# Optimization experiments

Hardware: AMD Instinct MI355X
Metric: run time of the kernel (lower is better)

Reference implementation:

```python
import jax, jax.numpy as jnp
import numpy as np

DIM = 1024
HEADS = 16
SCALE = DIM ** -0.5  # note: source scales by full dim, not head dim


def setup_inputs() -> dict:
    key = jax.random.key(0)
    k1, k2, k3 = jax.random.split(key, 3)
    b, n = 2, 2048
    x = jax.random.normal(k1, (b, n, DIM), dtype=jnp.float32)
    w_qkv = jax.random.normal(k2, (3 * DIM, DIM), dtype=jnp.float32) * (DIM ** -0.5)
    w_out = jax.random.normal(k3, (DIM, DIM), dtype=jnp.float32) * (DIM ** -0.5)
    b_out = jnp.zeros((DIM,), dtype=jnp.float32)
    return {"x": x, "w_qkv": w_qkv, "w_out": w_out, "b_out": b_out}


def reference(x, w_qkv, w_out, b_out):
    b, n, d = x.shape
    h = HEADS
    hd = d // h
    # torch Linear: y = x @ W.T
    qkv = x @ w_qkv.T  # [b, n, 3d]
    q, k, v = jnp.split(qkv, 3, axis=-1)
    # reshape to [b, h, n, hd]
    def to_heads(t):
        return t.reshape(b, n, h, hd).transpose(0, 2, 1, 3)
    q, k, v = to_heads(q), to_heads(k), to_heads(v)
    dots = jnp.einsum('bhqd,bhkd->bhqk', q, k) * SCALE
    attn = jax.nn.softmax(dots, axis=-1)
    out = jnp.einsum('bhqk,bhkd->bhqd', attn, v)
    out = out.transpose(0, 2, 1, 3).reshape(b, n, d)
    return out @ w_out.T + b_out
```

## Files before the change

### kernel.cpp

```cpp
#include <hip/hip_runtime.h>

typedef __attribute__((ext_vector_type(8))) _Float16 half8;
typedef __attribute__((ext_vector_type(4))) _Float16 half4;
typedef __attribute__((ext_vector_type(2))) __fp16 fp16x2;
typedef __attribute__((ext_vector_type(4))) float f32x4;
typedef __attribute__((ext_vector_type(4))) unsigned int u32x4;
typedef __attribute__((ext_vector_type(2))) unsigned int u32x2;

#define NSEQ 2048
#define DIMM 1024
#define NH   16
#define HD   64

typedef const void __attribute__((address_space(1))) gvoid_t;
typedef void __attribute__((address_space(3))) svoid_t;

__device__ __forceinline__ void gload_lds16(const void* g, void* l) {
  __builtin_amdgcn_global_load_lds((gvoid_t*)g, (svoid_t*)l, 16, 0, 0);
}

union H2U { fp16x2 h; unsigned int u; };

__global__ __launch_bounds__(256) void cvt_all(const float* __restrict__ x,
                                               const float* __restrict__ wqkv,
                                               const float* __restrict__ wout,
                                               _Float16* __restrict__ xh,
                                               _Float16* __restrict__ wqkvh,
                                               _Float16* __restrict__ wouth) {
  int i = blockIdx.x * 256 + threadIdx.x;
  const float* src;
  _Float16* dst;
  int off;
  if (i < 524288) { src = x; dst = xh; off = i; }
  else if (i < 917504) { src = wqkv; dst = wqkvh; off = i - 524288; }
  else { src = wout; dst = wouth; off = i - 917504; }
  const float4* p = (const float4*)src + (size_t)off * 2;
  float4 v0 = p[0], v1 = p[1];
  half8 h;
  h[0] = (_Float16)v0.x; h[1] = (_Float16)v0.y; h[2] = (_Float16)v0.z; h[3] = (_Float16)v0.w;
  h[4] = (_Float16)v1.x; h[5] = (_Float16)v1.y; h[6] = (_Float16)v1.z; h[7] = (_Float16)v1.w;
  *((half8*)dst + off) = h;
}

__device__ __forceinline__ void gemm_mainloop(const _Float16* __restrict__ A,
                                              const _Float16* __restrict__ B,
                                              int am0, int bn0,
                                              _Float16* As, _Float16* Bs,
                                              f32x4 acc[4][4]) {
  const int tid = threadIdx.x;
  const int w = tid >> 6, lane = tid & 63;
  const int lr = lane >> 2;
  const int lc = (lane & 3) * 8;
  const int wm = (w >> 1) * 64, wn = (w & 1) * 64;
  const int g = lane >> 4, ln = lane & 15;

  for (int k0 = 0; k0 < 1024; k0 += 32) {
#pragma unroll
    for (int rr = 0; rr < 4; ++rr) {
      int c = rr * 4 + w;
      if (c < 8) {
        gload_lds16(A + (size_t)(am0 + c * 16 + lr) * 1024 + k0 + lc, As + c * 512);
      } else {
        int cb = c - 8;
        gload_lds16(B + (size_t)(bn0 + cb * 16 + lr) * 1024 + k0 + lc, Bs + cb * 512);
      }
    }
    __syncthreads();
    half8 af[4], bf[4];
#pragma unroll
    for (int mi = 0; mi < 4; ++mi)
      af[mi] = *(const half8*)(As + (wm + mi * 16 + ln) * 32 + g * 8);
#pragma unroll
    for (int ni = 0; ni < 4; ++ni)
      bf[ni] = *(const half8*)(Bs + (wn + ni * 16 + ln) * 32 + g * 8);
#pragma unroll
    for (int mi = 0; mi < 4; ++mi)
#pragma unroll
      for (int ni = 0; ni < 4; ++ni)
        acc[mi][ni] = __builtin_amdgcn_mfma_f32_16x16x32_f16(af[mi], bf[ni], acc[mi][ni], 0, 0, 0);
    __syncthreads();
  }
}

union SmemQKV {
  struct { _Float16 a[128 * 32]; _Float16 b[128 * 32]; } ab;
  _Float16 t[128 * 136];
};

#define QSCALE 0.0450843450f

__global__ __launch_bounds__(256) void gemm_qkv(const _Float16* __restrict__ x,
                                                const _Float16* __restrict__ wqkv,
                                                _Float16* __restrict__ qh,
                                                _Float16* __restrict__ kh,
                                                _Float16* __restrict__ vt) {
  __shared__ SmemQKV sh;
  f32x4 acc[4][4];
#pragma unroll
  for (int i = 0; i < 4; ++i)
#pragma unroll
    for (int j = 0; j < 4; ++j) acc[i][j] = (f32x4){0.f, 0.f, 0.f, 0.f};
  const int bm = blockIdx.x, bn = blockIdx.y;
  gemm_mainloop(x, wqkv, bm * 128, bn * 128, sh.ab.a, sh.ab.b, acc);

  const int tid = threadIdx.x;
  const int w = tid >> 6, lane = tid & 63;
  const int g = lane >> 4, ln = lane & 15;
  const int wm = (w >> 1) * 64, wn = (w & 1) * 64;
  const int sec = bn >> 3;
  const int cbase = (bn & 7) * 128;

  if (sec < 2) {
    _Float16* dst = (sec == 0) ? qh : kh;
    const float scale = (sec == 0) ? QSCALE : 1.0f;
#pragma unroll
    for (int mi = 0; mi < 4; ++mi) {
      int row = bm * 128 + wm + mi * 16 + g * 4;
      int bidx = row >> 11, nidx = row & 2047;
#pragma unroll
      for (int ni = 0; ni < 4; ++ni) {
        int col = cbase + wn + ni * 16 + ln;
        int h = col >> 6, d = col & 63;
        _Float16* p = dst + ((size_t)(bidx * NH + h) * NSEQ + nidx) * HD + d;
#pragma unroll
        for (int r = 0; r < 4; ++r) p[r * HD] = (_Float16)(acc[mi][ni][r] * scale);
      }
    }
  } else {
    __syncthreads();
#pragma unroll
    for (int mi = 0; mi < 4; ++mi)
#pragma unroll
      for (int ni = 0; ni < 4; ++ni)
#pragma unroll
        for (int r = 0; r < 4; ++r)
          sh.t[(wn + ni * 16 + ln) * 136 + wm + mi * 16 + g * 4 + r] = (_Float16)acc[mi][ni][r];
    __syncthreads();
    const int row0 = bm * 128;
    const int bidx = row0 >> 11, n0 = row0 & 2047;
#pragma unroll
    for (int i = 0; i < 8; ++i) {
      int ci = i * 256 + tid;
      int drow = ci >> 4, nofs = (ci & 15) * 8;
      int col = cbase + drow;
      int h = col >> 6, d = col & 63;
      u32x4 val = *(const u32x4*)(sh.t + drow * 136 + nofs);
      *(u32x4*)(vt + ((size_t)(bidx * NH + h) * HD + d) * NSEQ + n0 + nofs) = val;
    }
  }
}

__global__ __launch_bounds__(256, 2) void attn_fwd(const _Float16* __restrict__ qg,
                                                   const _Float16* __restrict__ kg,
                                                   const _Float16* __restrict__ vg,
                                                   _Float16* __restrict__ ao) {
  __shared__ _Float16 Ks[3][64 * 64];
  __shared__ _Float16 Vs[3][64 * 64];
  __shared__ float Lred[2][128];

  const int bid = blockIdx.x;
  const int swz = (bid & 7) * 64 + (bid >> 3);
  const int bh = swz >> 4, qt = swz & 15;
  const int tid = threadIdx.x, w = tid >> 6, lane = tid & 63;
  const int g = lane >> 4, ln = lane & 15;
  const int sw8 = ln & 7;
  const int qh2 = w >> 1, kh2 = w & 1;

  const _Float16* qp = qg + (size_t)bh * NSEQ * HD;
  const _Float16* kp = kg + (size_t)bh * NSEQ * HD;
  const _Float16* vp = vg + (size_t)bh * HD * NSEQ;

  const int qr0 = qt * 128;

  half8 qf[4][2];
#pragma unroll
  for (int qb = 0; qb < 4; ++qb)
#pragma unroll
    for (int dk = 0; dk < 2; ++dk)
      qf[qb][dk] = *(const half8*)(qp + (size_t)(qr0 + qh2 * 64 + qb * 16 + ln) * HD + dk * 32 + g * 8);
  asm volatile("" ::: "memory");

  const int rsub = lane >> 3;
  const int csw = ((lane & 7) ^ rsub) << 3;
  const int c0 = 2 * w;
  const int R0 = c0 * 8 + rsub, R1 = R0 + 8;
  const int ks0 = 32 * (R0 >> 5) + 8 * ((R0 >> 2) & 3) + 4 * ((R0 >> 4) & 1) + (R0 & 3);
  const int ks1 = 32 * (R1 >> 5) + 8 * ((R1 >> 2) & 3) + 4 * ((R1 >> 4) & 1) + (R1 & 3);

#define STAGE(buf, tt)                                                              \
  {                                                                                 \
    const _Float16* kt_ = kp + (size_t)(tt) * 64 * HD;                              \
    gload_lds16(kt_ + (size_t)ks0 * HD + csw, &Ks[buf][c0 * 512]);                  \
    gload_lds16(kt_ + (size_t)ks1 * HD + csw, &Ks[buf][(c0 + 1) * 512]);            \
    gload_lds16(vp + (size_t)(c0 * 8 + rsub) * NSEQ + (tt) * 64 + csw,              \
                &Vs[buf][c0 * 512]);                                                \
    gload_lds16(vp + (size_t)((c0 + 1) * 8 + rsub) * NSEQ + (tt) * 64 + csw,        \
                &Vs[buf][(c0 + 1) * 512]);                                          \
  }

  STAGE(0, 0);
  STAGE(1, 1);

  float lsum[4] = {0.f, 0.f, 0.f, 0.f};
  f32x4 oacc[4][4];
#pragma unroll
  for (int sd = 0; sd < 4; ++sd)
#pragma unroll
    for (int qb = 0; qb < 4; ++qb) oacc[sd][qb] = (f32x4){0.f, 0.f, 0.f, 0.f};
  const f32x4 fz = (f32x4){0.f, 0.f, 0.f, 0.f};

#define TILE_BODY(kbuf, vbuf)                                                       \
  {                                                                                 \
    const _Float16* kb_ = (kbuf);                                                   \
    const _Float16* vb_ = (vbuf);                                                   \
    f32x4 sacc[2][4];                                                  \
    __builtin_amdgcn_s_setprio(1);                                                  \
    _Pragma("unroll")                                                               \
    for (int s = 0; s < 2; ++s) {                                                   \
      const _Float16* kr = kb_ + (kh2 * 32 + s * 16 + ln) * 64;                     \
      half8 kf0 = *(const half8*)(kr + ((g ^ sw8) << 3));                           \
      half8 kf1 = *(const half8*)(kr + (((4 + g) ^ sw8) << 3));                     \
      _Pragma("unroll")                                                             \
      for (int qb = 0; qb < 4; ++qb) {                                              \
        sacc[s][qb] = __builtin_amdgcn_mfma_f32_16x16x32_f16(kf0, qf[qb][0], fz, 0, 0, 0);          \
        sacc[s][qb] = __builtin_amdgcn_mfma_f32_16x16x32_f16(kf1, qf[qb][1], sacc[s][qb], 0, 0, 0); \
      }                                                                             \
    }                                                                               \
    __builtin_amdgcn_s_setprio(0);                                                  \
    half8 vf[4];                          \
    _Pragma("unroll")                                                               \
    for (int sd = 0; sd < 4; ++sd)                                                  \
      vf[sd] = *(const half8*)(vb_ + (sd * 16 + ln) * 64 +                          \
                               (((kh2 * 4 + g) ^ sw8) << 3));                       \
    half8 pb[4];                                                                    \
    _Pragma("unroll")                                                               \
    for (int qb = 0; qb < 4; ++qb) {                                                \
      float e0 = __builtin_amdgcn_exp2f(sacc[0][qb][0]);                            \
      float e1 = __builtin_amdgcn_exp2f(sacc[0][qb][1]);                            \
      float e2 = __builtin_amdgcn_exp2f(sacc[0][qb][2]);                            \
      float e3 = __builtin_amdgcn_exp2f(sacc[0][qb][3]);                            \
      float e4 = __builtin_amdgcn_exp2f(sacc[1][qb][0]);                            \
      float e5 = __builtin_amdgcn_exp2f(sacc[1][qb][1]);                            \
      float e6 = __builtin_amdgcn_exp2f(sacc[1][qb][2]);                            \
      float e7 = __builtin_amdgcn_exp2f(sacc[1][qb][3]);                            \
      lsum[qb] += ((e0 + e1) + (e2 + e3)) + ((e4 + e5) + (e6 + e7));                \
      H2U c0_, c1_, c2_, c3_;                                                       \
      c0_.h = __builtin_amdgcn_cvt_pkrtz(e0, e1);                                   \
      c1_.h = __builtin_amdgcn_cvt_pkrtz(e2, e3);                                   \
      c2_.h = __builtin_amdgcn_cvt_pkrtz(e4, e5);                                   \
      c3_.h = __builtin_amdgcn_cvt_pkrtz(e6, e7);                                   \
      union { u32x4 u; half8 h; } pk;                                               \
      pk.u[0] = c0_.u; pk.u[1] = c1_.u; pk.u[2] = c2_.u; pk.u[3] = c3_.u;           \
      pb[qb] = pk.h;                                                                \
    }                                                                               \
    __builtin_amdgcn_s_setprio(1);                                                  \
    _Pragma("unroll")                                                               \
    for (int sd = 0; sd < 4; ++sd)                                                  \
      _Pragma("unroll")                                                             \
      for (int qb = 0; qb < 4; ++qb)                                                \
        oacc[sd][qb] = __builtin_amdgcn_mfma_f32_16x16x32_f16(vf[sd], pb[qb], oacc[sd][qb], 0, 0, 0); \
    __builtin_amdgcn_s_setprio(0);                                                  \
  }

  for (int t = 0; t < 30; ++t) {
    asm volatile("s_waitcnt vmcnt(4)" ::: "memory");
    __builtin_amdgcn_s_barrier();
    STAGE((t + 2) % 3, t + 2);
    TILE_BODY(&Ks[t % 3][0], &Vs[t % 3][0])
  }
  {
    asm volatile("s_waitcnt vmcnt(4)" ::: "memory");
    __builtin_amdgcn_s_barrier();
    TILE_BODY(&Ks[0][0], &Vs[0][0])
  }
  {
    asm volatile("s_waitcnt vmcnt(0)" ::: "memory");
    __builtin_amdgcn_s_barrier();
    TILE_BODY(&Ks[1][0], &Vs[1][0])
  }

#pragma unroll
  for (int qb = 0; qb < 4; ++qb) {
    lsum[qb] += __shfl_xor(lsum[qb], 16, 64);
    lsum[qb] += __shfl_xor(lsum[qb], 32, 64);
  }
  __syncthreads();
  float* Osh = (float*)&Ks[0][0];
  if (g == 0) {
#pragma unroll
    for (int qb = 0; qb < 4; ++qb)
      Lred[kh2][qh2 * 64 + qb * 16 + ln] = lsum[qb];
  }
  if (kh2) {
#pragma unroll
    for (int sd = 0; sd < 4; ++sd)
#pragma unroll
      for (int qb = 0; qb < 4; ++qb)
        *(f32x4*)&Osh[(qh2 * 64 + qb * 16 + ln) * 66 + sd * 16 + g * 4] = oacc[sd][qb];
  }
  __syncthreads();
  if (!kh2) {
    const int bidx = bh >> 4, h = bh & 15;
#pragma unroll
    for (int qb = 0; qb < 4; ++qb) {
      const int q = qh2 * 64 + qb * 16 + ln;
      const float inv = 1.f / (Lred[0][q] + Lred[1][q]);
      const int n = qr0 + q;
#pragma unroll
      for (int sd = 0; sd < 4; ++sd) {
        f32x4 part = *(const f32x4*)&Osh[q * 66 + sd * 16 + g * 4];
        half4 o4;
#pragma unroll
        for (int r = 0; r < 4; ++r) o4[r] = (_Float16)((oacc[sd][qb][r] + part[r]) * inv);
        *(half4*)(ao + (size_t)(bidx * NSEQ + n) * DIMM + h * HD + sd * 16 + g * 4) = o4;
      }
    }
  }
}

__global__ __launch_bounds__(256) void gemm_out(const _Float16* __restrict__ ao,
                                                const _Float16* __restrict__ wout,
                                                const float* __restrict__ bias,
                                                float* __restrict__ out) {
  __shared__ _Float16 As[128 * 32];
  __shared__ _Float16 Bs[128 * 32];
  f32x4 acc[4][4];
#pragma unroll
  for (int i = 0; i < 4; ++i)
#pragma unroll
    for (int j = 0; j < 4; ++j) acc[i][j] = (f32x4){0.f, 0.f, 0.f, 0.f};
  const int bm = blockIdx.x, bn = blockIdx.y;
  gemm_mainloop(ao, wout, bm * 128, bn * 128, As, Bs, acc);
  const int tid = threadIdx.x;
  const int w = tid >> 6, lane = tid & 63;
  const int g = lane >> 4, ln = lane & 15;
  const int wm = (w >> 1) * 64, wn = (w & 1) * 64;
#pragma unroll
  for (int mi = 0; mi < 4; ++mi) {
    const int row = bm * 128 + wm + mi * 16 + g * 4;
#pragma unroll
    for (int ni = 0; ni < 4; ++ni) {
      const int col = bn * 128 + wn + ni * 16 + ln;
      const float b = bias[col];
#pragma unroll
      for (int r = 0; r < 4; ++r) out[(size_t)(row + r) * DIMM + col] = acc[mi][ni][r] + b;
    }
  }
}

extern "C" void kernel_launch(void* const* d_in, const int* in_sizes, int n_in,
                              void* d_out, int out_size, void* d_ws, size_t ws_size,
                              hipStream_t stream) {
  const float* x    = (const float*)d_in[0];
  const float* wqkv = (const float*)d_in[1];
  const float* wout = (const float*)d_in[2];
  const float* bout = (const float*)d_in[3];
  float* out = (float*)d_out;

  _Float16* ws = (_Float16*)d_ws;
  _Float16* x_h    = ws;
  _Float16* wqkv_h = ws + (4u << 20);
  _Float16* wout_h = ws + (7u << 20);
  _Float16* q_h    = ws + (8u << 20);
  _Float16* k_h    = ws + (12u << 20);
  _Float16* vt_h   = ws + (16u << 20);
  _Float16* ao_h   = ws + (20u << 20);

  cvt_all<<<dim3(4096), 256, 0, stream>>>(x, wqkv, wout, x_h, wqkv_h, wout_h);
  gemm_qkv<<<dim3(32, 24), 256, 0, stream>>>(x_h, wqkv_h, q_h, k_h, vt_h);
  attn_fwd<<<dim3(512), 256, 0, stream>>>(q_h, k_h, vt_h, ao_h);
  gemm_out<<<dim3(32, 8), 256, 0, stream>>>(ao_h, wout_h, bout, out);
}
```

Baseline: 108.2 us.

## Triple-buffer GEMM mainloops with async LDS loads and halve gemm_out N-tile

Both the QKV and output GEMM mainloops now use a three-stage LDS ring filled by global_load_lds, with explicit vmcnt waits and a single barrier per k-step. This lets the loads for step t+2 overlap the MFMAs of step t and replaces the two __syncthreads per iteration. The output projection GEMM also moves to a 128x64 tile, doubling its grid from 256 to 512 blocks for better CU occupancy on a small problem. The cost is more LDS per block, and correctness now depends on the hand-written vmcnt counts matching the number of loads each wave issues.

```diff
diff --git a/kernel.cpp b/kernel.cpp
--- a/kernel.cpp
+++ b/kernel.cpp
@@ -42,11 +42,11 @@
   *((half8*)dst + off) = h;
 }
 
-__device__ __forceinline__ void gemm_mainloop(const _Float16* __restrict__ A,
-                                              const _Float16* __restrict__ B,
-                                              int am0, int bn0,
-                                              _Float16* As, _Float16* Bs,
-                                              f32x4 acc[4][4]) {
+__device__ __forceinline__ void gemm_mainloop_q(const _Float16* __restrict__ A,
+                                                const _Float16* __restrict__ B,
+                                                int am0, int bn0,
+                                                _Float16* As, _Float16* Bs,
+                                                f32x4 acc[4][4]) {
   const int tid = threadIdx.x;
   const int w = tid >> 6, lane = tid & 63;
   const int lr = lane >> 2;
@@ -54,36 +54,51 @@
   const int wm = (w >> 1) * 64, wn = (w & 1) * 64;
   const int g = lane >> 4, ln = lane & 15;
 
-  for (int k0 = 0; k0 < 1024; k0 += 32) {
-#pragma unroll
-    for (int rr = 0; rr < 4; ++rr) {
-      int c = rr * 4 + w;
-      if (c < 8) {
-        gload_lds16(A + (size_t)(am0 + c * 16 + lr) * 1024 + k0 + lc, As + c * 512);
-      } else {
-        int cb = c - 8;
-        gload_lds16(B + (size_t)(bn0 + cb * 16 + lr) * 1024 + k0 + lc, Bs + cb * 512);
-      }
-    }
-    __syncthreads();
+#define GSTAGE_Q(buf, kk)                                                           \
+  {                                                                                 \
+    _Pragma("unroll")                                                               \
+    for (int i = 0; i < 4; ++i) {                                                   \
+      int c = w * 4 + i;                                                            \
+      if (c < 8) {                                                                  \
+        gload_lds16(A + (size_t)(am0 + c * 16 + lr) * 1024 + (kk) + lc,             \
+                    As + (buf) * 4096 + c * 512);                                   \
+      } else {                                                                      \
+        int cb = c - 8;                                                             \
+        gload_lds16(B + (size_t)(bn0 + cb * 16 + lr) * 1024 + (kk) + lc,            \
+                    Bs + (buf) * 4096 + cb * 512);                                  \
+      }                                                                             \
+    }                                                                               \
+  }
+
+  GSTAGE_Q(0, 0)
+  GSTAGE_Q(1, 32)
+  for (int t = 0; t < 32; ++t) {
+    if (t < 31) {
+      asm volatile("s_waitcnt vmcnt(4)" ::: "memory");
+    } else {
+      asm volatile("s_waitcnt vmcnt(0)" ::: "memory");
+    }
+    __builtin_amdgcn_s_barrier();
+    if (t < 30) GSTAGE_Q((t + 2) % 3, (t + 2) * 32);
+    const _Float16* as_ = As + (t % 3) * 4096;
+    const _Float16* bs_ = Bs + (t % 3) * 4096;
     half8 af[4], bf[4];
 #pragma unroll
     for (int mi = 0; mi < 4; ++mi)
-      af[mi] = *(const half8*)(As + (wm + mi * 16 + ln) * 32 + g * 8);
+      af[mi] = *(const half8*)(as_ + (wm + mi * 16 + ln) * 32 + g * 8);
 #pragma unroll
     for (int ni = 0; ni < 4; ++ni)
-      bf[ni] = *(const half8*)(Bs + (wn + ni * 16 + ln) * 32 + g * 8);
+      bf[ni] = *(const half8*)(bs_ + (wn + ni * 16 + ln) * 32 + g * 8);
 #pragma unroll
     for (int mi = 0; mi < 4; ++mi)
 #pragma unroll
       for (int ni = 0; ni < 4; ++ni)
         acc[mi][ni] = __builtin_amdgcn_mfma_f32_16x16x32_f16(af[mi], bf[ni], acc[mi][ni], 0, 0, 0);
-    __syncthreads();
   }
 }
 
 union SmemQKV {
-  struct { _Float16 a[128 * 32]; _Float16 b[128 * 32]; } ab;
+  struct { _Float16 a[3 * 128 * 32]; _Float16 b[3 * 128 * 32]; } ab;
   _Float16 t[128 * 136];
 };
 
@@ -101,7 +116,7 @@
 #pragma unroll
     for (int j = 0; j < 4; ++j) acc[i][j] = (f32x4){0.f, 0.f, 0.f, 0.f};
   const int bm = blockIdx.x, bn = blockIdx.y;
-  gemm_mainloop(x, wqkv, bm * 128, bn * 128, sh.ab.a, sh.ab.b, acc);
+  gemm_mainloop_q(x, wqkv, bm * 128, bn * 128, sh.ab.a, sh.ab.b, acc);
 
   const int tid = threadIdx.x;
   const int w = tid >> 6, lane = tid & 63;
@@ -213,7 +228,7 @@
   {                                                                                 \
     const _Float16* kb_ = (kbuf);                                                   \
     const _Float16* vb_ = (vbuf);                                                   \
-    f32x4 sacc[2][4];                                                  \
+    f32x4 sacc[2][4];                                                               \
     __builtin_amdgcn_s_setprio(1);                                                  \
     _Pragma("unroll")                                                               \
     for (int s = 0; s < 2; ++s) {                                                   \
@@ -227,7 +242,7 @@
       }                                                                             \
     }                                                                               \
     __builtin_amdgcn_s_setprio(0);                                                  \
-    half8 vf[4];                          \
+    half8 vf[4];                                                                    \
     _Pragma("unroll")                                                               \
     for (int sd = 0; sd < 4; ++sd)                                                  \
       vf[sd] = *(const half8*)(vb_ + (sd * 16 + ln) * 64 +                          \
@@ -322,25 +337,71 @@
                                                 const _Float16* __restrict__ wout,
                                                 const float* __restrict__ bias,
                                                 float* __restrict__ out) {
-  __shared__ _Float16 As[128 * 32];
-  __shared__ _Float16 Bs[128 * 32];
-  f32x4 acc[4][4];
+  __shared__ _Float16 As[3 * 128 * 32];
+  __shared__ _Float16 Bs[3 * 64 * 32];
+  f32x4 acc[4][2];
 #pragma unroll
   for (int i = 0; i < 4; ++i)
 #pragma unroll
-    for (int j = 0; j < 4; ++j) acc[i][j] = (f32x4){0.f, 0.f, 0.f, 0.f};
+    for (int j = 0; j < 2; ++j) acc[i][j] = (f32x4){0.f, 0.f, 0.f, 0.f};
   const int bm = blockIdx.x, bn = blockIdx.y;
-  gemm_mainloop(ao, wout, bm * 128, bn * 128, As, Bs, acc);
+  const int am0 = bm * 128, bn0 = bn * 64;
+
   const int tid = threadIdx.x;
   const int w = tid >> 6, lane = tid & 63;
+  const int lr = lane >> 2;
+  const int lc = (lane & 3) * 8;
+  const int wm = (w >> 1) * 64, wn = (w & 1) * 32;
   const int g = lane >> 4, ln = lane & 15;
-  const int wm = (w >> 1) * 64, wn = (w & 1) * 64;
+
+#define GSTAGE_O(buf, kk)                                                           \
+  {                                                                                 \
+    _Pragma("unroll")                                                               \
+    for (int i = 0; i < 3; ++i) {                                                   \
+      int c = w * 3 + i;                                                            \
+      if (c < 8) {                                                                  \
+        gload_lds16(ao + (size_t)(am0 + c * 16 + lr) * 1024 + (kk) + lc,            \
+                    As + (buf) * 4096 + c * 512);                                   \
+      } else {                                                                      \
+        int cb = c - 8;                                                             \
+        gload_lds16(wout + (size_t)(bn0 + cb * 16 + lr) * 1024 + (kk) + lc,         \
+                    Bs + (buf) * 2048 + cb * 512);                                  \
+      }                                                                             \
+    }                                                                               \
+  }
+
+  GSTAGE_O(0, 0)
+  GSTAGE_O(1, 32)
+  for (int t = 0; t < 32; ++t) {
+    if (t < 31) {
+      asm volatile("s_waitcnt vmcnt(3)" ::: "memory");
+    } else {
+      asm volatile("s_waitcnt vmcnt(0)" ::: "memory");
+    }
+    __builtin_amdgcn_s_barrier();
+    if (t < 30) GSTAGE_O((t + 2) % 3, (t + 2) * 32);
+    const _Float16* as_ = As + (t % 3) * 4096;
+    const _Float16* bs_ = Bs + (t % 3) * 2048;
+    half8 af[4], bf[2];
+#pragma unroll
+    for (int mi = 0; mi < 4; ++mi)
+      af[mi] = *(const half8*)(as_ + (wm + mi * 16 + ln) * 32 + g * 8);
+#pragma unroll
+    for (int ni = 0; ni < 2; ++ni)
+      bf[ni] = *(const half8*)(bs_ + (wn + ni * 16 + ln) * 32 + g * 8);
+#pragma unroll
+    for (int mi = 0; mi < 4; ++mi)
+#pragma unroll
+      for (int ni = 0; ni < 2; ++ni)
+        acc[mi][ni] = __builtin_amdgcn_mfma_f32_16x16x32_f16(af[mi], bf[ni], acc[mi][ni], 0, 0, 0);
+  }
+
 #pragma unroll
   for (int mi = 0; mi < 4; ++mi) {
     const int row = bm * 128 + wm + mi * 16 + g * 4;
 #pragma unroll
-    for (int ni = 0; ni < 4; ++ni) {
-      const int col = bn * 128 + wn + ni * 16 + ln;
+    for (int ni = 0; ni < 2; ++ni) {
+      const int col = bn * 64 + wn + ni * 16 + ln;
       const float b = bias[col];
 #pragma unroll
       for (int r = 0; r < 4; ++r) out[(size_t)(row + r) * DIMM + col] = acc[mi][ni][r] + b;
@@ -369,5 +430,5 @@
   cvt_all<<<dim3(4096), 256, 0, stream>>>(x, wqkv, wout, x_h, wqkv_h, wout_h);
   gemm_qkv<<<dim3(32, 24), 256, 0, stream>>>(x_h, wqkv_h, q_h, k_h, vt_h);
   attn_fwd<<<dim3(512), 256, 0, stream>>>(q_h, k_h, vt_h, ao_h);
-  gemm_out<<<dim3(32, 8), 256, 0, stream>>>(ao_h, wout_h, bout, out);
-}
+  gemm_out<<<dim3(32, 16), 256, 0, stream>>>(ao_h, wout_h, bout, out);
+}
```

Result: faster. 105.7 us (-2.3%).
